# Kernel optimization log

Hardware: AMD Instinct MI355X
Metric: run time of the kernel (lower is better)

Reference implementation:

```python
import jax, jax.numpy as jnp
import numpy as np

B, S, E, H, N = 16384, 256, 128, 128, 34  # batch, state_dim, reduced_lang_dim, mlp hidden, N_task
TEMP = 0.1
EPS = 1e-8  # torch cosine_similarity eps


def setup_inputs() -> dict:
    key = jax.random.key(0)
    ks = jax.random.split(key, 12)
    sc = 0.05
    return {
        "state": jax.random.normal(ks[0], (B, S), dtype=jnp.float32),
        "task_id": jax.random.randint(ks[1], (B,), 0, N),
        "prior": jax.random.normal(ks[2], (B, N), dtype=jnp.float32),
        # stacked weights of the 34 per-task MLPs (Linear(S,H) -> ReLU -> Linear(H,H) -> ReLU -> Linear(H,E))
        "W1": jax.random.normal(ks[3], (N, S, H), dtype=jnp.float32) * sc,
        "b1": jax.random.normal(ks[4], (N, H), dtype=jnp.float32) * sc,
        "W2": jax.random.normal(ks[5], (N, H, H), dtype=jnp.float32) * sc,
        "b2": jax.random.normal(ks[6], (N, H), dtype=jnp.float32) * sc,
        "W3": jax.random.normal(ks[7], (N, H, E), dtype=jnp.float32) * sc,
        "b3": jax.random.normal(ks[8], (N, E), dtype=jnp.float32) * sc,
        "lang_emb": jax.random.normal(ks[9], (N, E), dtype=jnp.float32),
    }


def reference(state, task_id, prior, W1, b1, W2, b2, W3, b3, lang_emb):
    # 34 parallel MLPs as a single batched GEMM stack: [B,S] x [N,S,H] -> [B,N,H]
    h = jax.nn.relu(jnp.einsum('bs,nsh->bnh', state, W1) + b1)
    h = jax.nn.relu(jnp.einsum('bnh,nhk->bnk', h, W2) + b2)
    q = jnp.einsum('bnk,nke->bne', h, W3) + b3            # [B,N,E]
    # normalize (torch.norm division, no eps, then cosine_similarity renormalizes -> unit)
    q = q / jnp.linalg.norm(q, axis=-1, keepdims=True)
    lang = lang_emb[task_id]                              # [B,E]
    lang_n = lang / jnp.maximum(jnp.linalg.norm(lang, axis=-1, keepdims=True), EPS)
    cos_sim = jnp.einsum('bne,be->bn', q, lang_n)         # [B,N]
    log_task_prob = jax.nn.log_softmax(cos_sim / TEMP, axis=-1)
    task_prob_prior = jax.nn.softmax(prior, axis=-1)      # exp(log_softmax(prior))
    latent_vec = jnp.einsum('bne,bn->be', q, task_prob_prior)
    latent_target = jax.lax.stop_gradient(q[jnp.arange(B), task_id])  # detach
    rep_vec = jnp.concatenate([state, latent_vec], axis=-1)           # [B, S+E]
    return rep_vec, log_task_prob, latent_target, latent_vec
```

## Files before the change

kernel.cpp:

```cpp
#include <hip/hip_runtime.h>
#include <hip/hip_bf16.h>
#include <hip/hip_fp16.h>
#include <cstdint>
#include <cstddef>

typedef __bf16 bf16;
typedef __attribute__((ext_vector_type(8))) __bf16 bf16x8;
typedef __attribute__((ext_vector_type(16))) float f32x16;

static_assert(sizeof(bf16x8) == 16, "bf16x8 must be 16B");

#define NTASK 34
#define BTOT 16384
#define WSTRIDE 73728

__device__ __forceinline__ f32x16 mfma32(bf16x8 a, bf16x8 b, f32x16 c) {
  return __builtin_amdgcn_mfma_f32_32x32x16_bf16(a, b, c, 0, 0, 0);
}

__device__ __forceinline__ void gload_lds16(const void* g, void* l) {
  __builtin_amdgcn_global_load_lds((__attribute__((address_space(1))) void*)g,
                                   (__attribute__((address_space(3))) void*)l,
                                   16, 0, 0);
}

__device__ __forceinline__ unsigned pack2(float lo, float hi) {
  union { __bf16 h[2]; unsigned u; } v;
  v.h[0] = (__bf16)lo; v.h[1] = (__bf16)hi;
  return v.u;
}

__device__ __forceinline__ void pl32swap(unsigned &a, unsigned &b) {
  asm volatile("v_permlane32_swap_b32 %0, %1" : "+v"(a), "+v"(b));
}

__global__ void prep_all(const float* __restrict__ W1, const float* __restrict__ W2,
                         const float* __restrict__ W3, const float* __restrict__ b1,
                         const float* __restrict__ b2, const float* __restrict__ b3,
                         const float* __restrict__ state, const float* __restrict__ prior,
                         bf16* __restrict__ wdst, bf16* __restrict__ sdst,
                         float* __restrict__ ppt) {
  int bid = blockIdx.x;
  if (bid < 1224) {
    int idx = bid * 256 + threadIdx.x;
    int n = idx / 9216;
    int r = idx - n * 9216;
    int g = r >> 8;
    int m = (r >> 6) & 3;
    int l = r & 63;
    int col = m * 32 + (l & 31);
    int kj = (l >> 5) << 3;
    bf16x8 v;
#pragma unroll
    for (int j = 0; j < 8; ++j) v[j] = (bf16)0.f;
    if (g < 16) {
      const float* s = W1 + ((size_t)n * 256 + g * 16 + kj) * 128 + col;
#pragma unroll
      for (int j = 0; j < 8; ++j) v[j] = (bf16)s[(size_t)j * 128];
    } else if (g == 16) {
      if (l < 32) v[0] = (bf16)b1[n * 128 + col];
    } else if (g == 17) {
    } else if (g < 26) {
      const float* s = W2 + ((size_t)n * 128 + (g - 18) * 16 + kj) * 128 + col;
#pragma unroll
      for (int j = 0; j < 8; ++j) v[j] = (bf16)s[(size_t)j * 128];
    } else if (g == 26) {
      if (l < 32) v[0] = (bf16)b2[n * 128 + col];
    } else if (g < 35) {
      const float* s = W3 + ((size_t)n * 128 + (g - 27) * 16 + kj) * 128 + col;
#pragma unroll
      for (int j = 0; j < 8; ++j) v[j] = (bf16)s[(size_t)j * 128];
    } else {
      if (l < 32) v[0] = (bf16)b3[n * 128 + col];
    }
    *(bf16x8*)(wdst + (size_t)n * WSTRIDE + (size_t)(g * 4 + m) * 512 + l * 8) = v;
  } else if (bid < 3272) {
    int idx = (bid - 1224) * 256 + threadIdx.x;
    int rb = idx >> 10;
    int r = idx & 1023;
    int ks = r >> 6;
    int l = r & 63;
    int b = rb * 32 + (l & 31);
    int k0 = ks * 16 + ((l >> 5) << 3);
    const float* s = state + (size_t)b * 256 + k0;
    bf16x8 v;
#pragma unroll
    for (int j = 0; j < 8; ++j) v[j] = (bf16)s[j];
    *(bf16x8*)(sdst + (size_t)(rb * 16 + ks) * 512 + l * 8) = v;
  } else {
    int row = (bid - 3272) * 4 + (threadIdx.x >> 6);
    int lane = threadIdx.x & 63;
    float v = (lane < NTASK) ? prior[(size_t)row * NTASK + lane] : -INFINITY;
    float m = v;
#pragma unroll
    for (int mm = 1; mm < 64; mm <<= 1) m = fmaxf(m, __shfl_xor(m, mm));
    float e = (lane < NTASK) ? expf(v - m) : 0.0f;
    float s = e;
#pragma unroll
    for (int mm = 1; mm < 64; mm <<= 1) s += __shfl_xor(s, mm);
    if (lane < NTASK) ppt[(size_t)lane * BTOT + row] = e / s;
  }
}

__global__ void prep_langn(const float* __restrict__ lang, float* __restrict__ out) {
  __shared__ float red[2];
  int n = blockIdx.x;
  int t = threadIdx.x;
  float v = lang[(size_t)n * 128 + t];
  float ss = v * v;
#pragma unroll
  for (int m = 1; m < 64; m <<= 1) ss += __shfl_xor(ss, m);
  if ((t & 63) == 0) red[t >> 6] = ss;
  __syncthreads();
  float s = red[0] + red[1];
  float sc = 1.0f / fmaxf(sqrtf(s), 1e-8f);
  out[(size_t)n * 128 + t] = v * sc;
}


__global__ void __launch_bounds__(256, 2)
pass1_kernel(const int* __restrict__ task_id, const bf16* __restrict__ wstream,
             const bf16* __restrict__ sf, const float* __restrict__ langn,
             const float* __restrict__ pp_t,
             float* __restrict__ cs_t, __half* __restrict__ lat_part,
             float* __restrict__ out_tgt) {
  __shared__ __align__(16) bf16 shW[3 * 8192];

  const int tid = threadIdx.x;
  const int l = tid & 63;
  const int wid = tid >> 6;
  const int hi = l >> 5;
  const int b = l & 31;
  const int tg = blockIdx.x >> 7;
  const int rg = blockIdx.x & 127;
  const int start = tg * 4 + (tg < 2 ? tg : 2);
  const int cnt = 4 + (tg < 2 ? 1 : 0);
  const int nwin = cnt * 9;
  const int row0 = rg * 128 + wid * 32 + b;
  const int rb0 = rg * 4 + wid;

  const int tidn = task_id[row0];
  const bf16* sb = sf + (size_t)rb0 * 8192 + l * 8;
  const bf16* wsrc = wstream + (size_t)start * WSTRIDE;

#define STAGE_WIN(slot, w) \
  { _Pragma("unroll") \
    for (int c = 0; c < 4; ++c) \
      gload_lds16(wsrc + (size_t)(w) * 8192 + c * 2048 + tid * 8, \
                  shW + (slot) * 8192 + c * 2048 + tid * 8); }

#define WIN_TOP(N) \
  { asm volatile("s_waitcnt vmcnt(" #N ")" ::: "memory"); \
    __builtin_amdgcn_s_barrier(); }

#define KMFMA(slot, gi, bop) \
  { _Pragma("unroll") \
    for (int mt = 0; mt < 4; ++mt) { \
      bf16x8 wf = *(const bf16x8*)(shW + (slot) * 8192 + ((gi) * 4 + mt) * 512 + l * 8); \
      acc[mt] = mfma32(wf, (bop), acc[mt]); } }

  STAGE_WIN(0, 0);
  STAGE_WIN(1, 1);
  bf16x8 sring[8];
#pragma unroll
  for (int i = 0; i < 8; ++i) sring[i] = *(const bf16x8*)(sb + i * 512);

  union { unsigned u[4]; bf16x8 v; } cf;
  cf.u[0] = (l < 32) ? 0x3f80u : 0u;
  cf.u[1] = 0u; cf.u[2] = 0u; cf.u[3] = 0u;

  f32x16 z;
#pragma unroll
  for (int i = 0; i < 16; ++i) z[i] = 0.f;
  f32x16 lat[4] = {z, z, z, z};

  auto transition = [&](f32x16* acc, bf16x8* f) {
#pragma unroll
    for (int mt = 0; mt < 4; ++mt) {
      unsigned p[8];
#pragma unroll
      for (int q = 0; q < 4; ++q) {
        p[2 * q]     = pack2(fmaxf(acc[mt][4 * q + 0], 0.f), fmaxf(acc[mt][4 * q + 1], 0.f));
        p[2 * q + 1] = pack2(fmaxf(acc[mt][4 * q + 2], 0.f), fmaxf(acc[mt][4 * q + 3], 0.f));
      }
      pl32swap(p[0], p[2]); pl32swap(p[1], p[3]);
      pl32swap(p[4], p[6]); pl32swap(p[5], p[7]);
      union { unsigned u[4]; bf16x8 v; } e, o;
      e.u[0] = p[0]; e.u[1] = p[1]; e.u[2] = p[2]; e.u[3] = p[3];
      o.u[0] = p[4]; o.u[1] = p[5]; o.u[2] = p[6]; o.u[3] = p[7];
      f[2 * mt] = e.v; f[2 * mt + 1] = o.v;
    }
  };

  for (int t = 0; t < cnt; ++t) {
    const int n = start + t;
    const int w0g = t * 9;
    f32x16 acc[4];
    bf16x8 f2[8], f3[8];

    WIN_TOP(12);
    if (w0g + 2 < nwin) STAGE_WIN(2, w0g + 2);
#pragma unroll
    for (int mt = 0; mt < 4; ++mt) acc[mt] = z;
    __builtin_amdgcn_s_setprio(1);
#pragma unroll
    for (int gi = 0; gi < 4; ++gi) KMFMA(0, gi, sring[gi]);
    __builtin_amdgcn_s_setprio(0);

    WIN_TOP(12);
    if (w0g + 3 < nwin) STAGE_WIN(0, w0g + 3);
#pragma unroll
    for (int i = 0; i < 4; ++i) sring[i] = *(const bf16x8*)(sb + (8 + i) * 512);
    __builtin_amdgcn_s_setprio(1);
#pragma unroll
    for (int gi = 0; gi < 4; ++gi) KMFMA(1, gi, sring[4 + gi]);
    __builtin_amdgcn_s_setprio(0);

    WIN_TOP(8);
    if (w0g + 4 < nwin) STAGE_WIN(1, w0g + 4);
#pragma unroll
    for (int i = 0; i < 4; ++i) sring[4 + i] = *(const bf16x8*)(sb + (12 + i) * 512);
    __builtin_amdgcn_s_setprio(1);
#pragma unroll
    for (int gi = 0; gi < 4; ++gi) KMFMA(2, gi, sring[gi]);
    __builtin_amdgcn_s_setprio(0);

    WIN_TOP(12);
    if (w0g + 5 < nwin) STAGE_WIN(2, w0g + 5);
    __builtin_amdgcn_s_setprio(1);
#pragma unroll
    for (int gi = 0; gi < 4; ++gi) KMFMA(0, gi, sring[4 + gi]);
    __builtin_amdgcn_s_setprio(0);

    WIN_TOP(8);
    if (w0g + 6 < nwin) STAGE_WIN(0, w0g + 6);
    __builtin_amdgcn_s_setprio(1);
    KMFMA(1, 0, cf.v);
    __builtin_amdgcn_s_setprio(0);
    transition(acc, f2);
#pragma unroll
    for (int mt = 0; mt < 4; ++mt) acc[mt] = z;
    __builtin_amdgcn_s_setprio(1);
    KMFMA(1, 2, f2[0]);
    KMFMA(1, 3, f2[1]);
    __builtin_amdgcn_s_setprio(0);

    WIN_TOP(4);
    if (w0g + 7 < nwin) STAGE_WIN(1, w0g + 7);
    __builtin_amdgcn_s_setprio(1);
#pragma unroll
    for (int gi = 0; gi < 4; ++gi) KMFMA(2, gi, f2[2 + gi]);
    __builtin_amdgcn_s_setprio(0);

    WIN_TOP(4);
    if (w0g + 8 < nwin) STAGE_WIN(2, w0g + 8);
    __builtin_amdgcn_s_setprio(1);
    KMFMA(0, 0, f2[6]);
    KMFMA(0, 1, f2[7]);
    KMFMA(0, 2, cf.v);
    __builtin_amdgcn_s_setprio(0);
    transition(acc, f3);
#pragma unroll
    for (int mt = 0; mt < 4; ++mt) acc[mt] = z;
    __builtin_amdgcn_s_setprio(1);
    KMFMA(0, 3, f3[0]);
    __builtin_amdgcn_s_setprio(0);

    WIN_TOP(4);
    if (w0g + 9 < nwin) STAGE_WIN(0, w0g + 9);
    __builtin_amdgcn_s_setprio(1);
#pragma unroll
    for (int gi = 0; gi < 4; ++gi) KMFMA(1, gi, f3[1 + gi]);
    __builtin_amdgcn_s_setprio(0);

    WIN_TOP(4);
    if (w0g + 10 < nwin) STAGE_WIN(1, w0g + 10);
    __builtin_amdgcn_s_setprio(1);
    KMFMA(2, 0, f3[5]);
    KMFMA(2, 1, f3[6]);
    KMFMA(2, 2, f3[7]);
    KMFMA(2, 3, cf.v);
    __builtin_amdgcn_s_setprio(0);

    if (t + 1 < cnt) {
#pragma unroll
      for (int i = 0; i < 8; ++i) sring[i] = *(const bf16x8*)(sb + i * 512);
    }

    float ssq = 0.f, dot = 0.f;
    const float* lgb = langn + (size_t)tidn * 128;
#pragma unroll
    for (int mt = 0; mt < 4; ++mt)
#pragma unroll
      for (int q = 0; q < 4; ++q) {
        int c0 = mt * 32 + q * 8 + 4 * hi;
        float4 lg = *(const float4*)(lgb + c0);
        float a0 = acc[mt][4 * q + 0], a1 = acc[mt][4 * q + 1];
        float a2 = acc[mt][4 * q + 2], a3 = acc[mt][4 * q + 3];
        ssq += a0 * a0 + a1 * a1 + a2 * a2 + a3 * a3;
        dot += a0 * lg.x + a1 * lg.y + a2 * lg.z + a3 * lg.w;
      }
    ssq += __shfl_xor(ssq, 32);
    dot += __shfl_xor(dot, 32);
    float inv = rsqrtf(ssq);
    if (l < 32) cs_t[(size_t)row0 * NTASK + n] = dot * inv;
    float pwi = pp_t[(size_t)n * BTOT + row0] * inv;
#pragma unroll
    for (int mt = 0; mt < 4; ++mt) lat[mt] += acc[mt] * pwi;
    if (tidn == n) {
#pragma unroll
      for (int mt = 0; mt < 4; ++mt)
#pragma unroll
        for (int q = 0; q < 4; ++q) {
          float4 qv = {acc[mt][4 * q + 0] * inv, acc[mt][4 * q + 1] * inv,
                       acc[mt][4 * q + 2] * inv, acc[mt][4 * q + 3] * inv};
          *(float4*)(out_tgt + (size_t)row0 * 128 + mt * 32 + q * 8 + 4 * hi) = qv;
        }
    }
  }

  __half* lp = lat_part + ((size_t)tg * BTOT + row0) * 128;
#pragma unroll
  for (int mt = 0; mt < 4; ++mt)
#pragma unroll
    for (int q = 0; q < 4; ++q) {
      int c0 = mt * 32 + q * 8 + 4 * hi;
      union { __half h[4]; uint2 u; } v;
      v.h[0] = __float2half(lat[mt][4 * q + 0]);
      v.h[1] = __float2half(lat[mt][4 * q + 1]);
      v.h[2] = __float2half(lat[mt][4 * q + 2]);
      v.h[3] = __float2half(lat[mt][4 * q + 3]);
      *(uint2*)(lp + c0) = v.u;
    }
#undef STAGE_WIN
#undef WIN_TOP
#undef KMFMA
}


__global__ void __launch_bounds__(256)
pass3_kernel(const float* __restrict__ state, const float* __restrict__ cs_t,
             const __half* __restrict__ lat_part,
             float* __restrict__ out_rep, float* __restrict__ out_ltp,
             float* __restrict__ out_lat) {
  int w = threadIdx.x >> 6, l = threadIdx.x & 63;
  size_t row = (size_t)blockIdx.x * 4 + w;

  float c = (l < NTASK) ? cs_t[row * NTASK + l] * 10.0f : -1e30f;
  float cm = c;
#pragma unroll
  for (int mm = 1; mm < 64; mm <<= 1) cm = fmaxf(cm, __shfl_xor(cm, mm));
  float ce = (l < NTASK) ? expf(c - cm) : 0.0f;
  float cs = ce;
#pragma unroll
  for (int mm = 1; mm < 64; mm <<= 1) cs += __shfl_xor(cs, mm);
  if (l < NTASK) out_ltp[row * NTASK + l] = c - cm - logf(cs);

  float2 lv = {0.f, 0.f};
#pragma unroll
  for (int g = 0; g < 8; ++g) {
    __half2 p = *(const __half2*)(lat_part + ((size_t)g * BTOT + row) * 128 + 2 * l);
    lv.x += __low2float(p);
    lv.y += __high2float(p);
  }
  *(float2*)(out_lat + row * 128 + 2 * l) = lv;
  *(float2*)(out_rep + row * 384 + 256 + 2 * l) = lv;

  float4 sv = *(const float4*)(state + row * 256 + l * 4);
  *(float4*)(out_rep + row * 384 + l * 4) = sv;
}


extern "C" void kernel_launch(void* const* d_in, const int* in_sizes, int n_in,
                              void* d_out, int out_size, void* d_ws, size_t ws_size,
                              hipStream_t stream) {
  (void)in_sizes; (void)n_in; (void)out_size; (void)ws_size;
  const float* state = (const float*)d_in[0];
  const int* task_id = (const int*)d_in[1];
  const float* prior = (const float*)d_in[2];
  const float* W1 = (const float*)d_in[3];
  const float* b1 = (const float*)d_in[4];
  const float* W2 = (const float*)d_in[5];
  const float* b2 = (const float*)d_in[6];
  const float* W3 = (const float*)d_in[7];
  const float* b3 = (const float*)d_in[8];
  const float* lang = (const float*)d_in[9];

  char* ws = (char*)d_ws;
  bf16* wstream  = (bf16*)(ws + 0);
  bf16* sf       = (bf16*)(ws + 5013504);
  float* langn   = (float*)(ws + 13402112);
  float* pp_t    = (float*)(ws + 13419520);
  float* cs_t    = (float*)(ws + 15647744);
  __half* lat_part = (__half*)(ws + 17875968);

  float* out = (float*)d_out;
  float* out_rep = out;
  float* out_ltp = out + 6291456;
  float* out_tgt = out + 6848512;
  float* out_lat = out + 8945664;

  prep_all<<<7368, 256, 0, stream>>>(W1, W2, W3, b1, b2, b3, state, prior,
                                     wstream, sf, pp_t);
  prep_langn<<<NTASK, 128, 0, stream>>>(lang, langn);
  pass1_kernel<<<1024, 256, 0, stream>>>(task_id, wstream, sf, langn, pp_t,
                                         cs_t, lat_part, out_tgt);
  pass3_kernel<<<4096, 256, 0, stream>>>(state, cs_t, lat_part,
                                         out_rep, out_ltp, out_lat);
}
```

Measured before the change: 145.1 us.

## Split tasks into four groups and keep full state tile in registers

Cuts the pass1 grid from 8 task groups to 4, so each block processes 8 or 9 tasks and the kernel launches 512 blocks instead of 1024. The full 16-fragment state tile is now kept in registers for all tasks, which removes the per-task reloads of state from global memory. The wait counts become a uniform vmcnt(4), and pass3 sums 4 latent partials instead of 8. The trade-offs are fewer blocks to fill the GPU, higher register pressure that could cause spills or lower occupancy, and less partial-sum traffic in the final pass.

Measured after the change: 133.6 us. -7.9%, faster.

```diff
diff --git a/kernel.cpp b/kernel.cpp
--- a/kernel.cpp
+++ b/kernel.cpp
@@ -133,8 +133,8 @@
   const int b = l & 31;
   const int tg = blockIdx.x >> 7;
   const int rg = blockIdx.x & 127;
-  const int start = tg * 4 + (tg < 2 ? tg : 2);
-  const int cnt = 4 + (tg < 2 ? 1 : 0);
+  const int start = (tg < 2) ? tg * 9 : (18 + (tg - 2) * 8);
+  const int cnt = (tg < 2) ? 9 : 8;
   const int nwin = cnt * 9;
   const int row0 = rg * 128 + wid * 32 + b;
   const int rb0 = rg * 4 + wid;
@@ -149,8 +149,8 @@
       gload_lds16(wsrc + (size_t)(w) * 8192 + c * 2048 + tid * 8, \
                   shW + (slot) * 8192 + c * 2048 + tid * 8); }
 
-#define WIN_TOP(N) \
-  { asm volatile("s_waitcnt vmcnt(" #N ")" ::: "memory"); \
+#define WIN_TOP() \
+  { asm volatile("s_waitcnt vmcnt(4)" ::: "memory"); \
     __builtin_amdgcn_s_barrier(); }
 
 #define KMFMA(slot, gi, bop) \
@@ -161,9 +161,9 @@
 
   STAGE_WIN(0, 0);
   STAGE_WIN(1, 1);
-  bf16x8 sring[8];
-#pragma unroll
-  for (int i = 0; i < 8; ++i) sring[i] = *(const bf16x8*)(sb + i * 512);
+  bf16x8 sring[16];
+#pragma unroll
+  for (int i = 0; i < 16; ++i) sring[i] = *(const bf16x8*)(sb + i * 512);
 
   union { unsigned u[4]; bf16x8 v; } cf;
   cf.u[0] = (l < 32) ? 0x3f80u : 0u;
@@ -198,7 +198,7 @@
     f32x16 acc[4];
     bf16x8 f2[8], f3[8];
 
-    WIN_TOP(12);
+    WIN_TOP();
     if (w0g + 2 < nwin) STAGE_WIN(2, w0g + 2);
 #pragma unroll
     for (int mt = 0; mt < 4; ++mt) acc[mt] = z;
@@ -207,32 +207,28 @@
     for (int gi = 0; gi < 4; ++gi) KMFMA(0, gi, sring[gi]);
     __builtin_amdgcn_s_setprio(0);
 
-    WIN_TOP(12);
+    WIN_TOP();
     if (w0g + 3 < nwin) STAGE_WIN(0, w0g + 3);
-#pragma unroll
-    for (int i = 0; i < 4; ++i) sring[i] = *(const bf16x8*)(sb + (8 + i) * 512);
     __builtin_amdgcn_s_setprio(1);
 #pragma unroll
     for (int gi = 0; gi < 4; ++gi) KMFMA(1, gi, sring[4 + gi]);
     __builtin_amdgcn_s_setprio(0);
 
-    WIN_TOP(8);
+    WIN_TOP();
     if (w0g + 4 < nwin) STAGE_WIN(1, w0g + 4);
-#pragma unroll
-    for (int i = 0; i < 4; ++i) sring[4 + i] = *(const bf16x8*)(sb + (12 + i) * 512);
-    __builtin_amdgcn_s_setprio(1);
-#pragma unroll
-    for (int gi = 0; gi < 4; ++gi) KMFMA(2, gi, sring[gi]);
-    __builtin_amdgcn_s_setprio(0);
-
-    WIN_TOP(12);
+    __builtin_amdgcn_s_setprio(1);
+#pragma unroll
+    for (int gi = 0; gi < 4; ++gi) KMFMA(2, gi, sring[8 + gi]);
+    __builtin_amdgcn_s_setprio(0);
+
+    WIN_TOP();
     if (w0g + 5 < nwin) STAGE_WIN(2, w0g + 5);
     __builtin_amdgcn_s_setprio(1);
 #pragma unroll
-    for (int gi = 0; gi < 4; ++gi) KMFMA(0, gi, sring[4 + gi]);
-    __builtin_amdgcn_s_setprio(0);
-
-    WIN_TOP(8);
+    for (int gi = 0; gi < 4; ++gi) KMFMA(0, gi, sring[12 + gi]);
+    __builtin_amdgcn_s_setprio(0);
+
+    WIN_TOP();
     if (w0g + 6 < nwin) STAGE_WIN(0, w0g + 6);
     __builtin_amdgcn_s_setprio(1);
     KMFMA(1, 0, cf.v);
@@ -245,14 +241,14 @@
     KMFMA(1, 3, f2[1]);
     __builtin_amdgcn_s_setprio(0);
 
-    WIN_TOP(4);
+    WIN_TOP();
     if (w0g + 7 < nwin) STAGE_WIN(1, w0g + 7);
     __builtin_amdgcn_s_setprio(1);
 #pragma unroll
     for (int gi = 0; gi < 4; ++gi) KMFMA(2, gi, f2[2 + gi]);
     __builtin_amdgcn_s_setprio(0);
 
-    WIN_TOP(4);
+    WIN_TOP();
     if (w0g + 8 < nwin) STAGE_WIN(2, w0g + 8);
     __builtin_amdgcn_s_setprio(1);
     KMFMA(0, 0, f2[6]);
@@ -266,14 +262,14 @@
     KMFMA(0, 3, f3[0]);
     __builtin_amdgcn_s_setprio(0);
 
-    WIN_TOP(4);
+    WIN_TOP();
     if (w0g + 9 < nwin) STAGE_WIN(0, w0g + 9);
     __builtin_amdgcn_s_setprio(1);
 #pragma unroll
     for (int gi = 0; gi < 4; ++gi) KMFMA(1, gi, f3[1 + gi]);
     __builtin_amdgcn_s_setprio(0);
 
-    WIN_TOP(4);
+    WIN_TOP();
     if (w0g + 10 < nwin) STAGE_WIN(1, w0g + 10);
     __builtin_amdgcn_s_setprio(1);
     KMFMA(2, 0, f3[5]);
@@ -281,11 +277,6 @@
     KMFMA(2, 2, f3[7]);
     KMFMA(2, 3, cf.v);
     __builtin_amdgcn_s_setprio(0);
-
-    if (t + 1 < cnt) {
-#pragma unroll
-      for (int i = 0; i < 8; ++i) sring[i] = *(const bf16x8*)(sb + i * 512);
-    }
 
     float ssq = 0.f, dot = 0.f;
     const float* lgb = langn + (size_t)tidn * 128;
@@ -358,7 +349,7 @@
 
   float2 lv = {0.f, 0.f};
 #pragma unroll
-  for (int g = 0; g < 8; ++g) {
+  for (int g = 0; g < 4; ++g) {
     __half2 p = *(const __half2*)(lat_part + ((size_t)g * BTOT + row) * 128 + 2 * l);
     lv.x += __low2float(p);
     lv.y += __high2float(p);
@@ -403,8 +394,8 @@
   prep_all<<<7368, 256, 0, stream>>>(W1, W2, W3, b1, b2, b3, state, prior,
                                      wstream, sf, pp_t);
   prep_langn<<<NTASK, 128, 0, stream>>>(lang, langn);
-  pass1_kernel<<<1024, 256, 0, stream>>>(task_id, wstream, sf, langn, pp_t,
-                                         cs_t, lat_part, out_tgt);
+  pass1_kernel<<<512, 256, 0, stream>>>(task_id, wstream, sf, langn, pp_t,
+                                        cs_t, lat_part, out_tgt);
   pass3_kernel<<<4096, 256, 0, stream>>>(state, cs_t, lat_part,
                                          out_rep, out_ltp, out_lat);
 }
```
